# Optimization experiments

Measured on AMD Instinct MI355X. Metric: run time of the kernel, lower is better.

## Reference

```python
import jax, jax.numpy as jnp
import numpy as np

B, N = 2, 8192

PARAM_SHAPES = {
    'down0_w': (32, 3), 'down0_b': (32,),
    'sc1_w1': (32, 35), 'sc1_b1': (32,), 'sc1_w2': (64, 32), 'sc1_b2': (64,),
    'sc2_w1': (64, 67), 'sc2_b1': (64,), 'sc2_w2': (128, 64), 'sc2_b2': (128,),
    'sc3_w1': (128, 131), 'sc3_b1': (128,), 'sc3_w2': (192, 128), 'sc3_b2': (192,),
    'sc4_w1': (192, 195), 'sc4_b1': (192,), 'sc4_w2': (192, 192), 'sc4_b2': (192,),
    'up4_w1': (192, 195), 'up4_b1': (192,), 'up4_w2': (192, 384), 'up4_b2': (192,),
    'up3_w1': (128, 195), 'up3_b1': (128,), 'up3_w2': (128, 256), 'up3_b2': (128,),
    'up2_w1': (64, 131), 'up2_b1': (64,), 'up2_w2': (64, 128), 'up2_b2': (64,),
    'up1_w1': (32, 67), 'up1_b1': (32,), 'up1_w2': (32, 64), 'up1_b2': (32,),
}
PNAMES = list(PARAM_SHAPES.keys())


def _fps(xyz, m):
    # xyz [N,3] -> [m] int32 farthest-point-sample indices (deterministic, start at point 0)
    def body(dmin, _):
        nxt = jnp.argmax(dmin)
        d = jnp.sum((xyz - xyz[nxt]) ** 2, -1)
        return jnp.minimum(dmin, d), nxt.astype(jnp.int32)
    d0 = jnp.sum((xyz - xyz[0]) ** 2, -1)
    _, rest = jax.lax.scan(body, d0, None, length=m - 1)
    return jnp.concatenate([jnp.zeros((1,), jnp.int32), rest])


def _gather(pts, idx):
    # pts [B,N,C], idx [B,...] -> [B,...,C]
    return jax.vmap(lambda p, i: p[i])(pts, idx)


def _ball_query(new_xyz, xyz, radius, k):
    # first-k points within radius, invalid slots filled with the first valid index
    d2 = jnp.sum((new_xyz[:, :, None, :] - xyz[:, None, :, :]) ** 2, -1)  # [B,M,N]
    n = xyz.shape[1]
    order = jnp.where(d2 <= radius * radius, jnp.arange(n)[None, None, :], n)
    idx = jnp.argsort(order, axis=-1)[..., :k]
    valid = jnp.take_along_axis(order, idx, -1) < n
    return jnp.where(valid, idx, idx[..., :1])


def _knn(query, ref, k):
    d2 = jnp.sum((query[:, :, None, :] - ref[:, None, :, :]) ** 2, -1)  # [B,Nq,Nr]
    _, idx = jax.lax.top_k(-d2, k)
    return idx


def _mlp(h, w, b):
    # pointwise shared MLP layer with ReLU on channel-last tensor
    return jax.nn.relu(jnp.einsum('...c,oc->...o', h, w) + b)


def _set_conv(xyz, feat, npoint, radius, k, w1, b1, w2, b2):
    # PointNet++-style SetConv: FPS -> ball-query group -> shared MLP -> max-pool
    fps_idx = jax.vmap(_fps, (0, None))(xyz, npoint)          # [B,M]
    new_xyz = _gather(xyz, fps_idx)                            # [B,M,3]
    gi = _ball_query(new_xyz, xyz, radius, k)                  # [B,M,k]
    h = jnp.concatenate([_gather(xyz, gi) - new_xyz[:, :, None, :], _gather(feat, gi)], -1)
    h = _mlp(_mlp(h, w1, b1), w2, b2)                          # [B,M,k,Cout]
    return new_xyz, fps_idx, jnp.max(h, axis=2)


def _set_upconv(s_xyz, d_xyz, s_feat, d_feat, k, w1, b1, w2, b2):
    # FlowNet3D-style SetUpConv: kNN from dense to sparse -> MLP -> max-pool -> fuse with dense feat
    gi = _knn(d_xyz, s_xyz, k)                                 # [B,Nd,k]
    h = jnp.concatenate([_gather(s_xyz, gi) - d_xyz[:, :, None, :], _gather(s_feat, gi)], -1)
    pooled = jnp.max(_mlp(h, w1, b1), axis=2)                  # [B,Nd,m1]
    return _mlp(jnp.concatenate([pooled, d_feat], -1), w2, b2)


def _encoder(pc, feat, p):
    xyz = jnp.transpose(pc, (0, 2, 1))                         # [B,N,3]
    f0 = _mlp(jnp.transpose(feat, (0, 2, 1)), p['down0_w'], p['down0_b'])  # [B,N,32]
    xyz1, i1, f1 = _set_conv(xyz, f0, 2048, 0.5, 16, p['sc1_w1'], p['sc1_b1'], p['sc1_w2'], p['sc1_b2'])
    xyz2, i2, f2 = _set_conv(xyz1, f1, 512, 1.0, 16, p['sc2_w1'], p['sc2_b1'], p['sc2_w2'], p['sc2_b2'])
    xyz3, i3, f3 = _set_conv(xyz2, f2, 128, 2.0, 16, p['sc3_w1'], p['sc3_b1'], p['sc3_w2'], p['sc3_b2'])
    xyz4, i4, f4 = _set_conv(xyz3, f3, 64, 4.0, 16, p['sc4_w1'], p['sc4_b1'], p['sc4_w2'], p['sc4_b2'])
    u3 = _set_upconv(xyz4, xyz3, f4, f3, 8, p['up4_w1'], p['up4_b1'], p['up4_w2'], p['up4_b2'])
    u2 = _set_upconv(xyz3, xyz2, u3, f2, 8, p['up3_w1'], p['up3_b1'], p['up3_w2'], p['up3_b2'])
    u1 = _set_upconv(xyz2, xyz1, u2, f1, 8, p['up2_w1'], p['up2_b1'], p['up2_w2'], p['up2_b2'])
    u0 = _set_upconv(xyz1, xyz, u1, f0, 8, p['up1_w1'], p['up1_b1'], p['up1_w2'], p['up1_b2'])
    return (xyz1, xyz2, xyz3), (i1, i2, i3), (u0, u1, u2, u3)


def setup_inputs() -> dict:
    key = jax.random.key(0)
    ks = jax.random.split(key, 2 + len(PNAMES))
    inp = {
        'pc': jax.random.normal(ks[0], (B, 3, N), jnp.float32),
        'feat': jax.random.normal(ks[1], (B, 3, N), jnp.float32),
    }
    for i, name in enumerate(PNAMES):
        inp[name] = jax.random.normal(ks[2 + i], PARAM_SHAPES[name], jnp.float32) * 0.05
    return inp


def reference(pc, feat, down0_w, down0_b, sc1_w1, sc1_b1, sc1_w2, sc1_b2, sc2_w1, sc2_b1, sc2_w2, sc2_b2, sc3_w1, sc3_b1, sc3_w2, sc3_b2, sc4_w1, sc4_b1, sc4_w2, sc4_b2, up4_w1, up4_b1, up4_w2, up4_b2, up3_w1, up3_b1, up3_w2, up3_b2, up2_w1, up2_b1, up2_w2, up2_b2, up1_w1, up1_b1, up1_w2, up1_b2):
    # GenFlow_unit.forward with gts[0] is None -> pure encoder path
    loc = locals()
    p = {k: loc[k] for k in PNAMES}
    (x1, x2, x3), (i1, i2, i3), (u0, u1, u2, u3) = _encoder(pc, feat, p)
    t = lambda a: jnp.transpose(a, (0, 2, 1))  # back to torch channel-first convention
    return (t(x1), t(x2), t(x3), i1, i2, i3, t(u0), t(u1), t(u2), t(u3))
```

## Files before the change

### kernel.cpp

```cpp
#include <hip/hip_runtime.h>
#include <hip/hip_bf16.h>
#include <cstdint>

#define DEV __device__ __forceinline__

DEV float sqdist(float ax, float ay, float az, float bx, float by, float bz) {
    float dx = __fsub_rn(ax, bx), dy = __fsub_rn(ay, by), dz = __fsub_rn(az, bz);
    return __fadd_rn(__fadd_rn(__fmul_rn(dx, dx), __fmul_rn(dy, dy)), __fmul_rn(dz, dz));
}

DEV unsigned short f2bf(float f) {
    unsigned int u = __float_as_uint(f);
    u += 0x7fffu + ((u >> 16) & 1u);
    return (unsigned short)(u >> 16);
}

DEV float bf2f(unsigned short u) { return __uint_as_float(((unsigned int)u) << 16); }

enum : int {
    O_X1 = 0, O_X2 = 12288, O_X3 = 15360,
    O_I1 = 16128, O_I2 = 20224, O_I3 = 21248,
    O_U0 = 21504, O_U1 = 545792, O_U2 = 807936, O_U3 = 939008
};

__global__ __launch_bounds__(256) void k_init(const float* __restrict__ pc,
                                              const float* __restrict__ feat,
                                              const float* __restrict__ w0,
                                              const float* __restrict__ b0,
                                              float* __restrict__ xyz,
                                              unsigned short* __restrict__ f0) {
    const int N = 8192;
    int i = blockIdx.x * blockDim.x + threadIdx.x;
    if (i >= 2 * N) return;
    int b = i / N, n = i % N;
    float fx0 = feat[(b * 3 + 0) * N + n];
    float fx1 = feat[(b * 3 + 1) * N + n];
    float fx2 = feat[(b * 3 + 2) * N + n];
    xyz[i * 3 + 0] = pc[(b * 3 + 0) * N + n];
    xyz[i * 3 + 1] = pc[(b * 3 + 1) * N + n];
    xyz[i * 3 + 2] = pc[(b * 3 + 2) * N + n];
#pragma unroll
    for (int o = 0; o < 32; o++) {
        float acc = b0[o];
        acc = fmaf(w0[o * 3 + 0], fx0, acc);
        acc = fmaf(w0[o * 3 + 1], fx1, acc);
        acc = fmaf(w0[o * 3 + 2], fx2, acc);
        f0[(size_t)i * 32 + o] = f2bf(fmaxf(acc, 0.f));
    }
}

template <int N, int M, int T>
__global__ __launch_bounds__(T, 1) void k_fps(const float* __restrict__ xyz,
                                              int* __restrict__ idx_out) {
    constexpr int P = N / T;
    constexpr int W = T / 64;
    int b = blockIdx.x;
    const float* X = xyz + (size_t)b * N * 3;
    int t = threadIdx.x;
    int w = t >> 6;
    __shared__ float sx[N], sy[N], sz[N];
    __shared__ unsigned long long skey[2][W];
    float px[P], py[P], pz[P], dmin[P];
    float c0x = X[0], c0y = X[1], c0z = X[2];
#pragma unroll
    for (int i = 0; i < P; i++) {
        int p = i * T + t;
        px[i] = X[p * 3 + 0];
        py[i] = X[p * 3 + 1];
        pz[i] = X[p * 3 + 2];
        sx[p] = px[i]; sy[p] = py[i]; sz[p] = pz[i];
        dmin[i] = sqdist(px[i], py[i], pz[i], c0x, c0y, c0z);
    }
    if (t == 0) idx_out[b * M] = 0;
    for (int j = 1; j < M; j++) {
        float mv[P];
#pragma unroll
        for (int i = 0; i < P; i++) mv[i] = dmin[i];
#pragma unroll
        for (int s = P / 2; s >= 1; s >>= 1)
#pragma unroll
            for (int i = 0; i < s; i++) mv[i] = fmaxf(mv[i], mv[i + s]);
        float bv = mv[0];
        int ii[P];
#pragma unroll
        for (int i = 0; i < P; i++) ii[i] = (dmin[i] == bv) ? (i * T + t) : 0x7fffffff;
#pragma unroll
        for (int s = P / 2; s >= 1; s >>= 1)
#pragma unroll
            for (int i = 0; i < s; i++) ii[i] = min(ii[i], ii[i + s]);
        unsigned long long key =
            ((unsigned long long)__float_as_uint(bv) << 32) | (unsigned int)~ii[0];
#pragma unroll
        for (int m = 1; m < 64; m <<= 1) {
            unsigned long long ok = __shfl_xor(key, m, 64);
            key = ok > key ? ok : key;
        }
        int sl = j & 1;
        if ((t & 63) == 0) skey[sl][w] = key;
        __syncthreads();
        unsigned long long gk = skey[sl][0];
#pragma unroll
        for (int u = 1; u < W; u++) {
            unsigned long long ok = skey[sl][u];
            gk = ok > gk ? ok : gk;
        }
        int gi = (int)~(unsigned int)gk;
        if (t == 0) idx_out[b * M + j] = gi;
        float cx = sx[gi], cy = sy[gi], cz = sz[gi];
#pragma unroll
        for (int i = 0; i < P; i++)
            dmin[i] = fminf(dmin[i], sqdist(px[i], py[i], pz[i], cx, cy, cz));
    }
}

__global__ __launch_bounds__(256) void k_gather(const float* __restrict__ xyz_src,
                                                const int* __restrict__ idx,
                                                float* __restrict__ xyz_dst,
                                                int NS, int M) {
    int i = blockIdx.x * blockDim.x + threadIdx.x;
    if (i >= 2 * M) return;
    int b = i / M;
    int id = idx[i] & (NS - 1);
    xyz_dst[i * 3 + 0] = xyz_src[((size_t)b * NS + id) * 3 + 0];
    xyz_dst[i * 3 + 1] = xyz_src[((size_t)b * NS + id) * 3 + 1];
    xyz_dst[i * 3 + 2] = xyz_src[((size_t)b * NS + id) * 3 + 2];
}

template <int NS, int CF, int CMID, int COUT>
__global__ __launch_bounds__(128) void k_setconv(
    const float* __restrict__ X, const unsigned short* __restrict__ F,
    const float* __restrict__ C, const float* __restrict__ w1,
    const float* __restrict__ b1, const float* __restrict__ w2,
    const float* __restrict__ b2, unsigned short* __restrict__ fout,
    float r2, int M) {
    constexpr int CIN = 3 + CF;
    constexpr int K = 16;
    constexpr int M8 = CMID / 8;
    constexpr int O8 = COUT / 8;
    int q = blockIdx.x, b = blockIdx.y;
    int blk = b * M + q;
    const float* Xb = X + (size_t)b * NS * 3;
    const unsigned short* Fb = F + (size_t)b * NS * CF;
    int tid = threadIdx.x;
    __shared__ int s_n[K];
    __shared__ int s_cnt;
    __shared__ float s_h[K][CIN];
    __shared__ float s_mid[K][CMID];
    __shared__ float s_pool[2][COUT];
    float cx = C[(size_t)blk * 3 + 0], cy = C[(size_t)blk * 3 + 1], cz = C[(size_t)blk * 3 + 2];
    if (tid < 64) {
        int lane = tid;
        int cnt = 0;
        for (int base = 0; base < NS; base += 64) {
            int p = base + lane;
            float d2 = sqdist(Xb[p * 3], Xb[p * 3 + 1], Xb[p * 3 + 2], cx, cy, cz);
            bool in = (d2 <= r2);
            unsigned long long msk = __ballot(in);
            if (in) {
                int pos = cnt + __popcll(msk & ((1ull << lane) - 1ull));
                if (pos < K) s_n[pos] = p;
            }
            cnt += __popcll(msk);
            if (cnt >= K) break;
        }
        if (lane == 0) s_cnt = cnt < K ? cnt : K;
    }
    __syncthreads();
    int cnt = s_cnt;
    if (tid >= cnt && tid < K) s_n[tid] = s_n[0];
    __syncthreads();
    for (int tIdx = tid; tIdx < K * CIN; tIdx += 128) {
        int n = tIdx / CIN, c = tIdx % CIN;
        int gi = s_n[n];
        float v;
        if (c < 3) v = __fsub_rn(Xb[gi * 3 + c], (c == 0 ? cx : (c == 1 ? cy : cz)));
        else v = bf2f(Fb[(size_t)gi * CF + (c - 3)]);
        s_h[n][c] = v;
    }
    __syncthreads();
    int n = tid >> 3, sub = tid & 7;
#pragma unroll
    for (int j = 0; j < M8; j++) {
        int m = sub * M8 + j;
        float acc = b1[m];
#pragma unroll 4
        for (int c = 0; c < CIN; c++) acc = fmaf(w1[m * CIN + c], s_h[n][c], acc);
        s_mid[n][m] = fmaxf(acc, 0.f);
    }
    __syncthreads();
    float vals[O8];
#pragma unroll
    for (int j = 0; j < O8; j++) {
        int o = sub * O8 + j;
        float acc = b2[o];
#pragma unroll 4
        for (int c = 0; c < CMID; c++) acc = fmaf(w2[o * CMID + c], s_mid[n][c], acc);
        vals[j] = fmaxf(acc, 0.f);
    }
#pragma unroll
    for (int j = 0; j < O8; j++) {
        vals[j] = fmaxf(vals[j], __shfl_xor(vals[j], 8, 64));
        vals[j] = fmaxf(vals[j], __shfl_xor(vals[j], 16, 64));
        vals[j] = fmaxf(vals[j], __shfl_xor(vals[j], 32, 64));
    }
    int lw = tid & 63, wv = tid >> 6;
    if (lw < 8) {
#pragma unroll
        for (int j = 0; j < O8; j++) s_pool[wv][lw * O8 + j] = vals[j];
    }
    __syncthreads();
    if (tid < 8) {
#pragma unroll
        for (int j = 0; j < O8; j++) {
            int o = tid * O8 + j;
            fout[(size_t)blk * COUT + o] = f2bf(fmaxf(s_pool[0][o], s_pool[1][o]));
        }
    }
}

template <int S, int CS, int CMID, int CD, int COUT, bool TRANS>
__global__ __launch_bounds__(64) void k_upconv(
    const float* __restrict__ SX, const float* __restrict__ DX,
    const void* __restrict__ SFv, const unsigned short* __restrict__ DF,
    const float* __restrict__ w1, const float* __restrict__ b1,
    const float* __restrict__ w2, const float* __restrict__ b2,
    float* __restrict__ out, int o_off, int ND) {
    constexpr int K = 8;
    constexpr int CIN = 3 + CS;
    constexpr int CIN2 = CMID + CD;
    constexpr int M8 = CMID / 8;
    int q = blockIdx.x, b = blockIdx.y;
    int blk = b * ND + q;
    int lane = threadIdx.x;
    const float* SXb = SX + (size_t)b * S * 3;
    float qx = DX[(size_t)blk * 3], qy = DX[(size_t)blk * 3 + 1], qz = DX[(size_t)blk * 3 + 2];
    __shared__ int s_k[K];
    __shared__ float s_h[K][CIN];
    __shared__ float s_in2[CIN2];
    float bd[K];
    int bi[K];
#pragma unroll
    for (int i = 0; i < K; i++) { bd[i] = 3.0e38f; bi[i] = 0x7fffffff; }
    for (int p = lane; p < S; p += 64) {
        float d2 = sqdist(SXb[p * 3], SXb[p * 3 + 1], SXb[p * 3 + 2], qx, qy, qz);
        if (d2 < bd[K - 1] || (d2 == bd[K - 1] && p < bi[K - 1])) {
            bd[K - 1] = d2; bi[K - 1] = p;
#pragma unroll
            for (int j = K - 1; j > 0; j--) {
                bool sw = (bd[j] < bd[j - 1]) || (bd[j] == bd[j - 1] && bi[j] < bi[j - 1]);
                if (sw) {
                    float tv = bd[j]; bd[j] = bd[j - 1]; bd[j - 1] = tv;
                    int ti = bi[j]; bi[j] = bi[j - 1]; bi[j - 1] = ti;
                }
            }
        }
    }
    for (int r = 0; r < K; r++) {
        float vv = bd[0]; int vi = bi[0];
#pragma unroll
        for (int m = 1; m < 64; m <<= 1) {
            float ov = __shfl_xor(vv, m, 64);
            int oi = __shfl_xor(vi, m, 64);
            if (ov < vv || (ov == vv && oi < vi)) { vv = ov; vi = oi; }
        }
        if (lane == 0) s_k[r] = vi;
        if (vi == bi[0]) {
#pragma unroll
            for (int j = 0; j < K - 1; j++) { bd[j] = bd[j + 1]; bi[j] = bi[j + 1]; }
            bd[K - 1] = 3.0e38f; bi[K - 1] = 0x7fffffff;
        }
    }
    __syncthreads();
    for (int tIdx = lane; tIdx < K * CIN; tIdx += 64) {
        int n = tIdx / CIN, c = tIdx % CIN;
        int gi = s_k[n];
        float v;
        if (c < 3) v = __fsub_rn(SXb[gi * 3 + c], (c == 0 ? qx : (c == 1 ? qy : qz)));
        else if (TRANS) v = ((const float*)SFv)[((size_t)b * CS + (c - 3)) * S + gi];
        else v = bf2f(((const unsigned short*)SFv)[((size_t)b * S + gi) * CS + (c - 3)]);
        s_h[n][c] = v;
    }
    for (int c = lane; c < CD; c += 64) s_in2[CMID + c] = bf2f(DF[(size_t)blk * CD + c]);
    __syncthreads();
    int n = lane >> 3, sub = lane & 7;
    float vals[M8];
#pragma unroll
    for (int j = 0; j < M8; j++) {
        int m = sub * M8 + j;
        float acc = b1[m];
#pragma unroll 4
        for (int c = 0; c < CIN; c++) acc = fmaf(w1[m * CIN + c], s_h[n][c], acc);
        vals[j] = fmaxf(acc, 0.f);
    }
#pragma unroll
    for (int j = 0; j < M8; j++) {
        vals[j] = fmaxf(vals[j], __shfl_xor(vals[j], 8, 64));
        vals[j] = fmaxf(vals[j], __shfl_xor(vals[j], 16, 64));
        vals[j] = fmaxf(vals[j], __shfl_xor(vals[j], 32, 64));
    }
    if (lane < 8) {
#pragma unroll
        for (int j = 0; j < M8; j++) s_in2[lane * M8 + j] = vals[j];
    }
    __syncthreads();
    for (int o = lane; o < COUT; o += 64) {
        float acc = b2[o];
#pragma unroll 4
        for (int c = 0; c < CIN2; c++) acc = fmaf(w2[o * CIN2 + c], s_in2[c], acc);
        out[o_off + ((size_t)b * COUT + o) * ND + q] = fmaxf(acc, 0.f);
    }
}

__global__ __launch_bounds__(256) void k_finalize(
    const float* __restrict__ xyz1, const float* __restrict__ xyz2,
    const float* __restrict__ xyz3, const int* __restrict__ idx1,
    const int* __restrict__ idx2, const int* __restrict__ idx3,
    float* __restrict__ out) {
    int i = blockIdx.x * blockDim.x + threadIdx.x;
    const float* xs;
    const int* is;
    int M, ox, oi, j;
    if (i < 4096) { xs = xyz1; is = idx1; M = 2048; ox = O_X1; oi = O_I1; j = i; }
    else if (i < 5120) { xs = xyz2; is = idx2; M = 512; ox = O_X2; oi = O_I2; j = i - 4096; }
    else if (i < 5376) { xs = xyz3; is = idx3; M = 128; ox = O_X3; oi = O_I3; j = i - 5120; }
    else return;
    int b = j / M, m = j % M;
    out[ox + (b * 3 + 0) * M + m] = xs[j * 3 + 0];
    out[ox + (b * 3 + 1) * M + m] = xs[j * 3 + 1];
    out[ox + (b * 3 + 2) * M + m] = xs[j * 3 + 2];
    out[oi + j] = (float)is[j];
}

extern "C" void kernel_launch(void* const* d_in, const int* in_sizes, int n_in,
                              void* d_out, int out_size, void* d_ws, size_t ws_size,
                              hipStream_t stream) {
    const float* pc = (const float*)d_in[0];
    const float* feat = (const float*)d_in[1];
    const float* w0 = (const float*)d_in[2];
    const float* b0v = (const float*)d_in[3];
    const float* sc1w1 = (const float*)d_in[4];  const float* sc1b1 = (const float*)d_in[5];
    const float* sc1w2 = (const float*)d_in[6];  const float* sc1b2 = (const float*)d_in[7];
    const float* sc2w1 = (const float*)d_in[8];  const float* sc2b1 = (const float*)d_in[9];
    const float* sc2w2 = (const float*)d_in[10]; const float* sc2b2 = (const float*)d_in[11];
    const float* sc3w1 = (const float*)d_in[12]; const float* sc3b1 = (const float*)d_in[13];
    const float* sc3w2 = (const float*)d_in[14]; const float* sc3b2 = (const float*)d_in[15];
    const float* sc4w1 = (const float*)d_in[16]; const float* sc4b1 = (const float*)d_in[17];
    const float* sc4w2 = (const float*)d_in[18]; const float* sc4b2 = (const float*)d_in[19];
    const float* up4w1 = (const float*)d_in[20]; const float* up4b1 = (const float*)d_in[21];
    const float* up4w2 = (const float*)d_in[22]; const float* up4b2 = (const float*)d_in[23];
    const float* up3w1 = (const float*)d_in[24]; const float* up3b1 = (const float*)d_in[25];
    const float* up3w2 = (const float*)d_in[26]; const float* up3b2 = (const float*)d_in[27];
    const float* up2w1 = (const float*)d_in[28]; const float* up2b1 = (const float*)d_in[29];
    const float* up2w2 = (const float*)d_in[30]; const float* up2b2 = (const float*)d_in[31];
    const float* up1w1 = (const float*)d_in[32]; const float* up1b1 = (const float*)d_in[33];
    const float* up1w2 = (const float*)d_in[34]; const float* up1b2 = (const float*)d_in[35];
    float* out = (float*)d_out;

    char* ws = (char*)d_ws;
    size_t off = 0;
    auto A = [&](size_t bytes) -> char* {
        char* p = ws + off;
        off += (bytes + 255) & ~(size_t)255;
        return p;
    };
    float* xyz  = (float*)A((size_t)2 * 8192 * 3 * 4);
    int* idx1   = (int*)A((size_t)2 * 2048 * 4);
    int* idx2   = (int*)A((size_t)2 * 512 * 4);
    int* idx3   = (int*)A((size_t)2 * 128 * 4);
    int* idx4   = (int*)A((size_t)2 * 64 * 4);
    float* xyz1 = (float*)A((size_t)2 * 2048 * 3 * 4);
    float* xyz2 = (float*)A((size_t)2 * 512 * 3 * 4);
    float* xyz3 = (float*)A((size_t)2 * 128 * 3 * 4);
    float* xyz4 = (float*)A((size_t)2 * 64 * 3 * 4);
    unsigned short* f0 = (unsigned short*)A((size_t)2 * 8192 * 32 * 2);
    unsigned short* f1 = (unsigned short*)A((size_t)2 * 2048 * 64 * 2);
    unsigned short* f2 = (unsigned short*)A((size_t)2 * 512 * 128 * 2);
    unsigned short* f3 = (unsigned short*)A((size_t)2 * 128 * 192 * 2);
    unsigned short* f4 = (unsigned short*)A((size_t)2 * 64 * 192 * 2);

    k_init<<<(2 * 8192 + 255) / 256, 256, 0, stream>>>(pc, feat, w0, b0v, xyz, f0);

    k_fps<8192, 2048, 512><<<2, 512, 0, stream>>>(xyz, idx1);
    k_gather<<<16, 256, 0, stream>>>(xyz, idx1, xyz1, 8192, 2048);
    k_setconv<8192, 32, 32, 64><<<dim3(2048, 2), 128, 0, stream>>>(
        xyz, f0, xyz1, sc1w1, sc1b1, sc1w2, sc1b2, f1, 0.25f, 2048);

    k_fps<2048, 512, 512><<<2, 512, 0, stream>>>(xyz1, idx2);
    k_gather<<<4, 256, 0, stream>>>(xyz1, idx2, xyz2, 2048, 512);
    k_setconv<2048, 64, 64, 128><<<dim3(512, 2), 128, 0, stream>>>(
        xyz1, f1, xyz2, sc2w1, sc2b1, sc2w2, sc2b2, f2, 1.0f, 512);

    k_fps<512, 128, 256><<<2, 256, 0, stream>>>(xyz2, idx3);
    k_gather<<<1, 256, 0, stream>>>(xyz2, idx3, xyz3, 512, 128);
    k_setconv<512, 128, 128, 192><<<dim3(128, 2), 128, 0, stream>>>(
        xyz2, f2, xyz3, sc3w1, sc3b1, sc3w2, sc3b2, f3, 4.0f, 128);

    k_fps<128, 64, 128><<<2, 128, 0, stream>>>(xyz3, idx4);
    k_gather<<<1, 128, 0, stream>>>(xyz3, idx4, xyz4, 128, 64);
    k_setconv<128, 192, 192, 192><<<dim3(64, 2), 128, 0, stream>>>(
        xyz3, f3, xyz4, sc4w1, sc4b1, sc4w2, sc4b2, f4, 16.0f, 64);

    k_upconv<64, 192, 192, 192, 192, false><<<dim3(128, 2), 64, 0, stream>>>(
        xyz4, xyz3, f4, f3, up4w1, up4b1, up4w2, up4b2, out, O_U3, 128);
    k_upconv<128, 192, 128, 128, 128, true><<<dim3(512, 2), 64, 0, stream>>>(
        xyz3, xyz2, out + O_U3, f2, up3w1, up3b1, up3w2, up3b2, out, O_U2, 512);
    k_upconv<512, 128, 64, 64, 64, true><<<dim3(2048, 2), 64, 0, stream>>>(
        xyz2, xyz1, out + O_U2, f1, up2w1, up2b1, up2w2, up2b2, out, O_U1, 2048);
    k_upconv<2048, 64, 32, 32, 32, true><<<dim3(8192, 2), 64, 0, stream>>>(
        xyz1, xyz, out + O_U1, f0, up1w1, up1b1, up1w2, up1b2, out, O_U0, 8192);

    k_finalize<<<(5376 + 255) / 256, 256, 0, stream>>>(
        xyz1, xyz2, xyz3, idx1, idx2, idx3, out);
}
```

Baseline: 4.460 ms.

## Use DPP wave reductions and halve FPS block sizes with single-wave sync-free path

Replaces the 64-bit shuffle-xor key reduction in FPS, and the argmin in kNN, with a float/int argmax/argmin pair reduction whose first four steps use DPP row operations instead of ds_bpermute shuffles. FPS blocks are halved in thread count, so each thread holds twice as many points. The smallest level becomes a single wave that skips the LDS exchange and __syncthreads entirely. This targets the serial per-iteration latency of the FPS loop, which dominates runtime, at the cost of more per-thread register work. The max-pool reductions in the setconv and upconv kernels also switch their first shuffle step to DPP.

```diff
diff --git a/kernel.cpp b/kernel.cpp
--- a/kernel.cpp
+++ b/kernel.cpp
@@ -16,6 +16,34 @@
 }
 
 DEV float bf2f(unsigned short u) { return __uint_as_float(((unsigned int)u) << 16); }
+
+template <int CTRL>
+DEV int dpp_i(int v) { return __builtin_amdgcn_update_dpp(v, v, CTRL, 0xf, 0xf, false); }
+template <int CTRL>
+DEV float dpp_f(float v) { return __int_as_float(dpp_i<CTRL>(__float_as_int(v))); }
+
+DEV void comb_max(float& v, int& i, float ov, int oi) {
+    if (ov > v || (ov == v && oi < i)) { v = ov; i = oi; }
+}
+DEV void comb_min(float& v, int& i, float ov, int oi) {
+    if (ov < v || (ov == v && oi < i)) { v = ov; i = oi; }
+}
+DEV void wave_argmax(float& v, int& i) {
+    comb_max(v, i, dpp_f<0x128>(v), dpp_i<0x128>(i));
+    comb_max(v, i, dpp_f<0x124>(v), dpp_i<0x124>(i));
+    comb_max(v, i, dpp_f<0x122>(v), dpp_i<0x122>(i));
+    comb_max(v, i, dpp_f<0x121>(v), dpp_i<0x121>(i));
+    comb_max(v, i, __shfl_xor(v, 16, 64), __shfl_xor(i, 16, 64));
+    comb_max(v, i, __shfl_xor(v, 32, 64), __shfl_xor(i, 32, 64));
+}
+DEV void wave_argmin(float& v, int& i) {
+    comb_min(v, i, dpp_f<0x128>(v), dpp_i<0x128>(i));
+    comb_min(v, i, dpp_f<0x124>(v), dpp_i<0x124>(i));
+    comb_min(v, i, dpp_f<0x122>(v), dpp_i<0x122>(i));
+    comb_min(v, i, dpp_f<0x121>(v), dpp_i<0x121>(i));
+    comb_min(v, i, __shfl_xor(v, 16, 64), __shfl_xor(i, 16, 64));
+    comb_min(v, i, __shfl_xor(v, 32, 64), __shfl_xor(i, 32, 64));
+}
 
 enum : int {
     O_X1 = 0, O_X2 = 12288, O_X3 = 15360,
@@ -59,7 +87,7 @@
     int t = threadIdx.x;
     int w = t >> 6;
     __shared__ float sx[N], sy[N], sz[N];
-    __shared__ unsigned long long skey[2][W];
+    __shared__ unsigned long long skey[2][W > 1 ? W : 1];
     float px[P], py[P], pz[P], dmin[P];
     float c0x = X[0], c0y = X[1], c0z = X[2];
 #pragma unroll
@@ -72,6 +100,7 @@
         dmin[i] = sqdist(px[i], py[i], pz[i], c0x, c0y, c0z);
     }
     if (t == 0) idx_out[b * M] = 0;
+    if constexpr (W == 1) __builtin_amdgcn_s_waitcnt(0);
     for (int j = 1; j < M; j++) {
         float mv[P];
 #pragma unroll
@@ -83,28 +112,30 @@
         float bv = mv[0];
         int ii[P];
 #pragma unroll
-        for (int i = 0; i < P; i++) ii[i] = (dmin[i] == bv) ? (i * T + t) : 0x7fffffff;
+        for (int i = 0; i < P; i++) ii[i] = (dmin[i] == bv) ? i : 0x7fffffff;
 #pragma unroll
         for (int s = P / 2; s >= 1; s >>= 1)
 #pragma unroll
             for (int i = 0; i < s; i++) ii[i] = min(ii[i], ii[i + s]);
-        unsigned long long key =
-            ((unsigned long long)__float_as_uint(bv) << 32) | (unsigned int)~ii[0];
-#pragma unroll
-        for (int m = 1; m < 64; m <<= 1) {
-            unsigned long long ok = __shfl_xor(key, m, 64);
-            key = ok > key ? ok : key;
+        int bi = (ii[0] == 0x7fffffff) ? 0x7fffffff : ii[0] * T + t;
+        wave_argmax(bv, bi);
+        int gi;
+        if constexpr (W > 1) {
+            unsigned long long key =
+                ((unsigned long long)__float_as_uint(bv) << 32) | (unsigned int)~bi;
+            int sl = j & 1;
+            if ((t & 63) == 0) skey[sl][w] = key;
+            __syncthreads();
+            unsigned long long gk = skey[sl][0];
+#pragma unroll
+            for (int u = 1; u < W; u++) {
+                unsigned long long ok = skey[sl][u];
+                gk = ok > gk ? ok : gk;
+            }
+            gi = (int)~(unsigned int)gk;
+        } else {
+            gi = bi;
         }
-        int sl = j & 1;
-        if ((t & 63) == 0) skey[sl][w] = key;
-        __syncthreads();
-        unsigned long long gk = skey[sl][0];
-#pragma unroll
-        for (int u = 1; u < W; u++) {
-            unsigned long long ok = skey[sl][u];
-            gk = ok > gk ? ok : gk;
-        }
-        int gi = (int)~(unsigned int)gk;
         if (t == 0) idx_out[b * M + j] = gi;
         float cx = sx[gi], cy = sy[gi], cz = sz[gi];
 #pragma unroll
@@ -199,7 +230,7 @@
     }
 #pragma unroll
     for (int j = 0; j < O8; j++) {
-        vals[j] = fmaxf(vals[j], __shfl_xor(vals[j], 8, 64));
+        vals[j] = fmaxf(vals[j], dpp_f<0x128>(vals[j]));
         vals[j] = fmaxf(vals[j], __shfl_xor(vals[j], 16, 64));
         vals[j] = fmaxf(vals[j], __shfl_xor(vals[j], 32, 64));
     }
@@ -257,12 +288,7 @@
     }
     for (int r = 0; r < K; r++) {
         float vv = bd[0]; int vi = bi[0];
-#pragma unroll
-        for (int m = 1; m < 64; m <<= 1) {
-            float ov = __shfl_xor(vv, m, 64);
-            int oi = __shfl_xor(vi, m, 64);
-            if (ov < vv || (ov == vv && oi < vi)) { vv = ov; vi = oi; }
-        }
+        wave_argmin(vv, vi);
         if (lane == 0) s_k[r] = vi;
         if (vi == bi[0]) {
 #pragma unroll
@@ -294,7 +320,7 @@
     }
 #pragma unroll
     for (int j = 0; j < M8; j++) {
-        vals[j] = fmaxf(vals[j], __shfl_xor(vals[j], 8, 64));
+        vals[j] = fmaxf(vals[j], dpp_f<0x128>(vals[j]));
         vals[j] = fmaxf(vals[j], __shfl_xor(vals[j], 16, 64));
         vals[j] = fmaxf(vals[j], __shfl_xor(vals[j], 32, 64));
     }
@@ -380,22 +406,22 @@
 
     k_init<<<(2 * 8192 + 255) / 256, 256, 0, stream>>>(pc, feat, w0, b0v, xyz, f0);
 
-    k_fps<8192, 2048, 512><<<2, 512, 0, stream>>>(xyz, idx1);
+    k_fps<8192, 2048, 256><<<2, 256, 0, stream>>>(xyz, idx1);
     k_gather<<<16, 256, 0, stream>>>(xyz, idx1, xyz1, 8192, 2048);
     k_setconv<8192, 32, 32, 64><<<dim3(2048, 2), 128, 0, stream>>>(
         xyz, f0, xyz1, sc1w1, sc1b1, sc1w2, sc1b2, f1, 0.25f, 2048);
 
-    k_fps<2048, 512, 512><<<2, 512, 0, stream>>>(xyz1, idx2);
+    k_fps<2048, 512, 256><<<2, 256, 0, stream>>>(xyz1, idx2);
     k_gather<<<4, 256, 0, stream>>>(xyz1, idx2, xyz2, 2048, 512);
     k_setconv<2048, 64, 64, 128><<<dim3(512, 2), 128, 0, stream>>>(
         xyz1, f1, xyz2, sc2w1, sc2b1, sc2w2, sc2b2, f2, 1.0f, 512);
 
-    k_fps<512, 128, 256><<<2, 256, 0, stream>>>(xyz2, idx3);
+    k_fps<512, 128, 128><<<2, 128, 0, stream>>>(xyz2, idx3);
     k_gather<<<1, 256, 0, stream>>>(xyz2, idx3, xyz3, 512, 128);
     k_setconv<512, 128, 128, 192><<<dim3(128, 2), 128, 0, stream>>>(
         xyz2, f2, xyz3, sc3w1, sc3b1, sc3w2, sc3b2, f3, 4.0f, 128);
 
-    k_fps<128, 64, 128><<<2, 128, 0, stream>>>(xyz3, idx4);
+    k_fps<128, 64, 64><<<2, 64, 0, stream>>>(xyz3, idx4);
     k_gather<<<1, 128, 0, stream>>>(xyz3, idx4, xyz4, 128, 64);
     k_setconv<128, 192, 192, 192><<<dim3(64, 2), 128, 0, stream>>>(
         xyz3, f3, xyz4, sc4w1, sc4b1, sc4w2, sc4b2, f4, 16.0f, 64);
```

Measured after the change: 4.791 ms. +7.4%, slower.

## Vectorize FPS distance math with packed float2 and use shared atomicMax reduction

Applied to the files above, without the earlier changes.

The farthest-point-sampling kernel now holds its points as float2 pairs so the distance and min/max updates can map to packed FP32 instructions. The cross-wave argmax uses a shared-memory atomicMax on a triple-buffered key instead of a per-wave slot array plus a serial scan. The smallest FPS level launches a single wave, which removes block synchronization entirely. The goal is to shorten the latency of each serial FPS iteration, at the cost of atomic contention and more complex buffer rotation.

```diff
diff --git a/kernel.cpp b/kernel.cpp
--- a/kernel.cpp
+++ b/kernel.cpp
@@ -4,9 +4,17 @@
 
 #define DEV __device__ __forceinline__
 
+typedef float f32x2 __attribute__((ext_vector_type(2)));
+
 DEV float sqdist(float ax, float ay, float az, float bx, float by, float bz) {
     float dx = __fsub_rn(ax, bx), dy = __fsub_rn(ay, by), dz = __fsub_rn(az, bz);
     return __fadd_rn(__fadd_rn(__fmul_rn(dx, dx), __fmul_rn(dy, dy)), __fmul_rn(dz, dz));
+}
+
+DEV f32x2 sqdist2(f32x2 ax, f32x2 ay, f32x2 az, float bx, float by, float bz) {
+#pragma clang fp contract(off)
+    f32x2 dx = ax - bx, dy = ay - by, dz = az - bz;
+    return (dx * dx + dy * dy) + dz * dz;
 }
 
 DEV unsigned short f2bf(float f) {
@@ -53,63 +61,73 @@
 __global__ __launch_bounds__(T, 1) void k_fps(const float* __restrict__ xyz,
                                               int* __restrict__ idx_out) {
     constexpr int P = N / T;
+    constexpr int P2 = P / 2;
     constexpr int W = T / 64;
     int b = blockIdx.x;
     const float* X = xyz + (size_t)b * N * 3;
     int t = threadIdx.x;
-    int w = t >> 6;
     __shared__ float sx[N], sy[N], sz[N];
-    __shared__ unsigned long long skey[2][W];
-    float px[P], py[P], pz[P], dmin[P];
+    __shared__ unsigned long long skey[3];
+    f32x2 px[P2], py[P2], pz[P2], dmin[P2];
     float c0x = X[0], c0y = X[1], c0z = X[2];
 #pragma unroll
-    for (int i = 0; i < P; i++) {
-        int p = i * T + t;
-        px[i] = X[p * 3 + 0];
-        py[i] = X[p * 3 + 1];
-        pz[i] = X[p * 3 + 2];
-        sx[p] = px[i]; sy[p] = py[i]; sz[p] = pz[i];
-        dmin[i] = sqdist(px[i], py[i], pz[i], c0x, c0y, c0z);
-    }
-    if (t == 0) idx_out[b * M] = 0;
+    for (int i = 0; i < P2; i++) {
+        int p0 = (2 * i) * T + t, p1 = (2 * i + 1) * T + t;
+        px[i] = f32x2{X[p0 * 3 + 0], X[p1 * 3 + 0]};
+        py[i] = f32x2{X[p0 * 3 + 1], X[p1 * 3 + 1]};
+        pz[i] = f32x2{X[p0 * 3 + 2], X[p1 * 3 + 2]};
+        sx[p0] = px[i].x; sy[p0] = py[i].x; sz[p0] = pz[i].x;
+        sx[p1] = px[i].y; sy[p1] = py[i].y; sz[p1] = pz[i].y;
+        dmin[i] = sqdist2(px[i], py[i], pz[i], c0x, c0y, c0z);
+    }
+    if (t == 0) {
+        idx_out[b * M] = 0;
+        skey[0] = 0; skey[1] = 0; skey[2] = 0;
+    }
+    __syncthreads();
+    int jm = 1;
     for (int j = 1; j < M; j++) {
-        float mv[P];
-#pragma unroll
-        for (int i = 0; i < P; i++) mv[i] = dmin[i];
+        f32x2 m2[P2];
+#pragma unroll
+        for (int i = 0; i < P2; i++) m2[i] = dmin[i];
+#pragma unroll
+        for (int s = P2 / 2; s >= 1; s >>= 1)
+#pragma unroll
+            for (int i = 0; i < s; i++) m2[i] = __builtin_elementwise_max(m2[i], m2[i + s]);
+        float bv = fmaxf(m2[0].x, m2[0].y);
+        int ii[P];
+#pragma unroll
+        for (int i = 0; i < P; i++)
+            ii[i] = (dmin[i >> 1][i & 1] == bv) ? (i * T + t) : 0x7fffffff;
 #pragma unroll
         for (int s = P / 2; s >= 1; s >>= 1)
 #pragma unroll
-            for (int i = 0; i < s; i++) mv[i] = fmaxf(mv[i], mv[i + s]);
-        float bv = mv[0];
-        int ii[P];
-#pragma unroll
-        for (int i = 0; i < P; i++) ii[i] = (dmin[i] == bv) ? (i * T + t) : 0x7fffffff;
-#pragma unroll
-        for (int s = P / 2; s >= 1; s >>= 1)
-#pragma unroll
             for (int i = 0; i < s; i++) ii[i] = min(ii[i], ii[i + s]);
+        int bi = ii[0];
         unsigned long long key =
-            ((unsigned long long)__float_as_uint(bv) << 32) | (unsigned int)~ii[0];
+            ((unsigned long long)__float_as_uint(bv) << 32) | (unsigned int)~bi;
 #pragma unroll
         for (int m = 1; m < 64; m <<= 1) {
             unsigned long long ok = __shfl_xor(key, m, 64);
             key = ok > key ? ok : key;
         }
-        int sl = j & 1;
-        if ((t & 63) == 0) skey[sl][w] = key;
-        __syncthreads();
-        unsigned long long gk = skey[sl][0];
-#pragma unroll
-        for (int u = 1; u < W; u++) {
-            unsigned long long ok = skey[sl][u];
-            gk = ok > gk ? ok : gk;
-        }
-        int gi = (int)~(unsigned int)gk;
+        int gi;
+        if constexpr (W > 1) {
+            if ((t & 63) == 0) atomicMax(&skey[jm], key);
+            __syncthreads();
+            unsigned long long gk = skey[jm];
+            gi = (int)~(unsigned int)gk;
+            if (t == 0) skey[jm == 0 ? 2 : jm - 1] = 0;
+            jm = (jm == 2) ? 0 : jm + 1;
+        } else {
+            gi = bi;
+        }
         if (t == 0) idx_out[b * M + j] = gi;
         float cx = sx[gi], cy = sy[gi], cz = sz[gi];
 #pragma unroll
-        for (int i = 0; i < P; i++)
-            dmin[i] = fminf(dmin[i], sqdist(px[i], py[i], pz[i], cx, cy, cz));
+        for (int i = 0; i < P2; i++)
+            dmin[i] = __builtin_elementwise_min(
+                dmin[i], sqdist2(px[i], py[i], pz[i], cx, cy, cz));
     }
 }
 
@@ -395,7 +413,7 @@
     k_setconv<512, 128, 128, 192><<<dim3(128, 2), 128, 0, stream>>>(
         xyz2, f2, xyz3, sc3w1, sc3b1, sc3w2, sc3b2, f3, 4.0f, 128);
 
-    k_fps<128, 64, 128><<<2, 128, 0, stream>>>(xyz3, idx4);
+    k_fps<128, 64, 64><<<2, 64, 0, stream>>>(xyz3, idx4);
     k_gather<<<1, 128, 0, stream>>>(xyz3, idx4, xyz4, 128, 64);
     k_setconv<128, 192, 192, 192><<<dim3(64, 2), 128, 0, stream>>>(
         xyz3, f3, xyz4, sc4w1, sc4b1, sc4w2, sc4b2, f4, 16.0f, 64);
```

Result: slower. 4.557 ms (+2.2%).
